# Optimization experiments

Measured on AMD Instinct MI355X. Metric: run time of the kernel, lower is better.

## Reference

```python
import jax, jax.numpy as jnp
import numpy as np

NUM_HEADS = 8
MASK_RATE = 0.5


def setup_inputs() -> dict:
    key = jax.random.key(0)
    ks = jax.random.split(key, 6)
    B, N, C = 8, 1024, 256
    TABLE = 10
    att_embedding = jax.random.normal(ks[0], (B, N, C), dtype=jnp.float32)
    relation_position = jax.random.randint(ks[1], (B, N, N), 0, TABLE, dtype=jnp.int32)
    rel_len = jax.random.randint(ks[2], (B,), 0, 20, dtype=jnp.int32)
    W_qkv = jax.random.normal(ks[3], (C, 3 * C), dtype=jnp.float32) * (1.0 / np.sqrt(C))
    W_proj = jax.random.normal(ks[4], (C, C), dtype=jnp.float32) * (1.0 / np.sqrt(C))
    b_proj = jnp.zeros((C,), dtype=jnp.float32)
    bias_table = jax.random.normal(ks[5], (TABLE, NUM_HEADS), dtype=jnp.float32) * 0.02
    return {
        "att_embedding": att_embedding,
        "relation_position": relation_position,
        "rel_len": rel_len,
        "W_qkv": W_qkv,
        "W_proj": W_proj,
        "b_proj": b_proj,
        "bias_table": bias_table,
    }


def reference(att_embedding, relation_position, rel_len, W_qkv, W_proj, b_proj, bias_table):
    B, N, C = att_embedding.shape
    H = NUM_HEADS
    hd = C // H
    scale = hd ** -0.5

    # QKV projection (no bias): [B,N,3C] -> q,k,v each [B,H,N,hd]
    qkv = (att_embedding @ W_qkv).reshape(B, N, 3, H, hd)
    qkv = jnp.transpose(qkv, (2, 0, 3, 1, 4))
    q, k, v = qkv[0], qkv[1], qkv[2]

    # Attention scores [B,H,N,N]
    attn = jnp.einsum("bhnd,bhmd->bhnm", q, k) * scale

    # Relative position bias: gather [B,N,N,H] -> [B,H,N,N]
    pos_bias = jnp.transpose(bias_table[relation_position], (0, 3, 1, 2))

    # Mask bias: table row t gets -100 iff t > mask_len (mask_len+1 .. TABLE-1);
    # identical across heads -> compute as [B,1,N,N] instead of materializing [B,H,N,N].
    mask_len = (rel_len.astype(jnp.float32) * MASK_RATE).astype(jnp.int32)
    mask_bias = jnp.where(relation_position > mask_len[:, None, None], -100.0, 0.0)[:, None]

    attn = jax.nn.softmax(attn + pos_bias + mask_bias, axis=-1)

    # Weighted values -> [B,N,C] -> output projection
    x = jnp.einsum("bhnm,bhmd->bnhd", attn, v).reshape(B, N, C)
    x = x @ W_proj + b_proj
    return x
```

## Files before the change

### kernel.cpp

```cpp
#include <hip/hip_runtime.h>
#include <hip/hip_bf16.h>

typedef __bf16 bf16;
typedef __bf16 bf16x2 __attribute__((ext_vector_type(2)));
typedef __bf16 bf16x8 __attribute__((ext_vector_type(8)));
typedef float f32x4 __attribute__((ext_vector_type(4)));
typedef int i32x4 __attribute__((ext_vector_type(4)));

#define B_ 8
#define N_ 1024
#define C_ 256
#define H_ 8
#define C3_ 768
#define QS 0.25500398f
#define FMAX 16.0f


__global__ __launch_bounds__(256) void prep(
    const float* __restrict__ Wqkv, const float* __restrict__ Wproj,
    bf16* __restrict__ Wq_tiled, bf16* __restrict__ Wp_tiled)
{
  int bb = blockIdx.x;
  int o = bb * 256 + threadIdx.x;
  if (bb < 768) {
    int kk = o & 31;
    int idx = o >> 5;
    int nr = idx & 63;
    int qq = idx >> 6;
    int nt = qq % 12, kt = qq / 12;
    int n = nt * 64 + nr, k = kt * 32 + kk;
    Wq_tiled[o] = (bf16)Wqkv[k * C3_ + n];
  } else {
    int p = o - 768 * 256;
    int kk = p & 31;
    int n = (p >> 5) & 255;
    int kt = p >> 13;
    int k = kt * 32 + kk;
    Wp_tiled[p] = (bf16)Wproj[k * C_ + n];
  }
}

__global__ __launch_bounds__(256) void gemm_qkv(
    const float* __restrict__ A, const bf16* __restrict__ Wq_tiled,
    bf16* __restrict__ q, bf16* __restrict__ kT, bf16* __restrict__ vT)
{
  __shared__ bf16 As[128][40];
  __shared__ bf16 Bts[128][40];
  __shared__ bf16 Vls[64][136];

  int tid = threadIdx.x;
  int wave = tid >> 6, lane = tid & 63, quad = lane >> 4, l16 = lane & 15;
  int m0 = blockIdx.x * 128, n0 = blockIdx.y * 128;
  int msub = (wave & 1) * 64, nsub = (wave >> 1) * 64;

  f32x4 acc[4][4] = {};

  int arow = tid >> 1, akc = (tid & 1) * 16;
  const float* aptr = A + (long)(m0 + arow) * C_ + akc;
  int bn = tid >> 1, bkc = (tid & 1) * 16;
  const bf16* bptr = Wq_tiled +
      ((long)(blockIdx.y * 2 + (bn >> 6)) * 2048 + (bn & 63) * 32 + bkc);

  float4 a0 = *reinterpret_cast<const float4*>(aptr);
  float4 a1 = *reinterpret_cast<const float4*>(aptr + 4);
  float4 a2 = *reinterpret_cast<const float4*>(aptr + 8);
  float4 a3 = *reinterpret_cast<const float4*>(aptr + 12);
  i32x4 bv0 = *reinterpret_cast<const i32x4*>(bptr);
  i32x4 bv1 = *reinterpret_cast<const i32x4*>(bptr + 8);

  for (int kt = 0; kt < 8; ++kt) {
    __syncthreads();
    {
      bf16 at[16] = {(bf16)a0.x, (bf16)a0.y, (bf16)a0.z, (bf16)a0.w,
                     (bf16)a1.x, (bf16)a1.y, (bf16)a1.z, (bf16)a1.w,
                     (bf16)a2.x, (bf16)a2.y, (bf16)a2.z, (bf16)a2.w,
                     (bf16)a3.x, (bf16)a3.y, (bf16)a3.z, (bf16)a3.w};
      *reinterpret_cast<bf16x8*>(&As[arow][akc]) = *reinterpret_cast<bf16x8*>(at);
      *reinterpret_cast<bf16x8*>(&As[arow][akc + 8]) = *reinterpret_cast<bf16x8*>(at + 8);
      *reinterpret_cast<i32x4*>(&Bts[bn][bkc]) = bv0;
      *reinterpret_cast<i32x4*>(&Bts[bn][bkc + 8]) = bv1;
    }
    __syncthreads();

    if (kt < 7) {
      int kn = (kt + 1) * 32;
      a0 = *reinterpret_cast<const float4*>(aptr + kn);
      a1 = *reinterpret_cast<const float4*>(aptr + kn + 4);
      a2 = *reinterpret_cast<const float4*>(aptr + kn + 8);
      a3 = *reinterpret_cast<const float4*>(aptr + kn + 12);
      bv0 = *reinterpret_cast<const i32x4*>(bptr + (long)(kt + 1) * 24576);
      bv1 = *reinterpret_cast<const i32x4*>(bptr + (long)(kt + 1) * 24576 + 8);
    }

    bf16x8 af[4], bfr[4];
#pragma unroll
    for (int mi = 0; mi < 4; ++mi)
      af[mi] = *reinterpret_cast<const bf16x8*>(&As[msub + mi * 16 + l16][quad * 8]);
#pragma unroll
    for (int ni = 0; ni < 4; ++ni)
      bfr[ni] = *reinterpret_cast<const bf16x8*>(&Bts[nsub + ni * 16 + l16][quad * 8]);
#pragma unroll
    for (int mi = 0; mi < 4; ++mi)
#pragma unroll
      for (int ni = 0; ni < 4; ++ni)
        acc[mi][ni] = __builtin_amdgcn_mfma_f32_16x16x32_bf16(af[mi], bfr[ni], acc[mi][ni], 0, 0, 0);
  }

  if (n0 < 256) {
#pragma unroll
    for (int mi = 0; mi < 4; ++mi)
#pragma unroll
      for (int ni = 0; ni < 4; ++ni)
#pragma unroll
        for (int r = 0; r < 4; ++r) {
          int row = m0 + msub + mi * 16 + quad * 4 + r;
          int col = n0 + nsub + ni * 16 + l16;
          q[(long)row * 256 + col] = (bf16)(acc[mi][ni][r] * QS);
        }
  } else if (n0 < 512) {
#pragma unroll
    for (int mi = 0; mi < 4; ++mi)
#pragma unroll
      for (int ni = 0; ni < 4; ++ni)
#pragma unroll
        for (int r = 0; r < 4; ++r) {
          int row = m0 + msub + mi * 16 + quad * 4 + r;
          int c = n0 + nsub + ni * 16 + l16 - 256;
          int b = row >> 10, n = row & 1023;
          int h = c >> 5, d = c & 31;
          kT[(((long)(b * H_ + h)) * N_ + n) * 32 + d] = (bf16)acc[mi][ni][r];
        }
  } else {
    int b = m0 >> 10;
#pragma unroll
    for (int ch = 0; ch < 2; ++ch) {
      __syncthreads();
      if ((nsub >> 6) == ch) {
#pragma unroll
        for (int mi = 0; mi < 4; ++mi)
#pragma unroll
          for (int ni = 0; ni < 4; ++ni)
#pragma unroll
            for (int r = 0; r < 4; ++r) {
              int cc = ni * 16 + l16;
              int nn = msub + mi * 16 + quad * 4 + r;
              int np = (nn & 96) | (2 * (nn & 15)) | ((nn >> 4) & 1);
              Vls[cc][np] = (bf16)acc[mi][ni][r];
            }
      }
      __syncthreads();
      int cc = tid >> 2, nseg = (tid & 3) * 32;
      long base = ((long)(b * C_ + (n0 - 512) + ch * 64 + cc)) * N_ + (m0 & 1023) + nseg;
#pragma unroll
      for (int j = 0; j < 4; ++j)
        *reinterpret_cast<i32x4*>(vT + base + j * 8) =
            *reinterpret_cast<const i32x4*>(&Vls[cc][nseg + j * 8]);
    }
  }
}

__global__ __launch_bounds__(512) void flash_attn(
    const bf16* __restrict__ q, const bf16* __restrict__ kT,
    const bf16* __restrict__ vT, const int* __restrict__ rel,
    const int* __restrict__ rel_len, const float* __restrict__ btab,
    const bf16* __restrict__ Wp_tiled, const float* __restrict__ bias,
    float* __restrict__ out)
{
  __shared__ bf16 Vs[H_][32][40];
  __shared__ bf16 Pls[H_][16 * 40];
  __shared__ float btlq[4][H_][17];
  __shared__ bf16 attL[16][264];

  int tid = threadIdx.x;
  int h = tid >> 6, lane = tid & 63, quad = lane >> 4, l16 = lane & 15;
  int b = blockIdx.y, i0 = blockIdx.x * 16;
  long bN = (long)b * N_;

  int mask_len = (int)((float)rel_len[b] * 0.5f);
  if (tid < 320) {
    int cp = tid / 80, rem = tid % 80, t = rem >> 3, hh = rem & 7;
    btlq[cp][hh][t] =
        (btab[t * H_ + hh] + (t > mask_len ? -100.f : 0.f) - FMAX) * 1.44269504f;
  }
  __syncthreads();

  bf16x8 qf = *reinterpret_cast<const bf16x8*>(
      q + (bN + i0 + l16) * 256 + h * 32 + quad * 8);

  const bf16* kbase = kT + ((long)(b * H_ + h)) * N_ * 32 + quad * 8;
  int vrl = lane >> 1, voff = (lane & 1) * 16;
  const bf16* vgp = vT + ((long)b * C_ + h * 32 + vrl) * N_ + voff;
  const int* relr = rel + (bN + i0 + quad * 4) * N_ + l16;

  bf16x8 kf0 = *reinterpret_cast<const bf16x8*>(kbase + (long)l16 * 32);
  bf16x8 kf1 = *reinterpret_cast<const bf16x8*>(kbase + (long)(16 + l16) * 32);
  bf16x8 vr0 = *reinterpret_cast<const bf16x8*>(vgp);
  bf16x8 vr1 = *reinterpret_cast<const bf16x8*>(vgp + 8);
  int rv[8];
#pragma unroll
  for (int r = 0; r < 4; ++r) {
    rv[r] = relr[(long)r * N_];
    rv[4 + r] = relr[(long)r * N_ + 16];
  }

  f32x4 oacc[2] = {};
  float l_part[4] = {0.f, 0.f, 0.f, 0.f};

  for (int j0 = 0; j0 < N_; j0 += 32) {
    *reinterpret_cast<bf16x8*>(&Vs[h][vrl][voff]) = vr0;
    *reinterpret_cast<bf16x8*>(&Vs[h][vrl][voff + 8]) = vr1;

    int jn = j0 + 32; jn = (jn < N_) ? jn : 0;
    bf16x8 kn0 = *reinterpret_cast<const bf16x8*>(kbase + (long)(jn + l16) * 32);
    bf16x8 kn1 = *reinterpret_cast<const bf16x8*>(kbase + (long)(jn + 16 + l16) * 32);
    bf16x8 vn0 = *reinterpret_cast<const bf16x8*>(vgp + jn);
    bf16x8 vn1 = *reinterpret_cast<const bf16x8*>(vgp + jn + 8);
    int rn[8];
#pragma unroll
    for (int r = 0; r < 4; ++r) {
      rn[r] = relr[(long)r * N_ + jn];
      rn[4 + r] = relr[(long)r * N_ + jn + 16];
    }

    f32x4 z = {};
    f32x4 s0 = __builtin_amdgcn_mfma_f32_16x16x32_bf16(qf, kf0, z, 0, 0, 0);
    f32x4 s1 = __builtin_amdgcn_mfma_f32_16x16x32_bf16(qf, kf1, z, 0, 0, 0);
    kf0 = kn0; kf1 = kn1;

#pragma unroll
    for (int r = 0; r < 4; ++r) {
      int il = quad * 4 + r;
      float p0 = exp2f(s0[r] + btlq[quad][h][rv[r]]);
      float p1 = exp2f(s1[r] + btlq[quad][h][rv[4 + r]]);
      l_part[r] += p0 + p1;
      bf16x2 pp = {(bf16)p0, (bf16)p1};
      *reinterpret_cast<bf16x2*>(&Pls[h][il * 40 + l16 * 2]) = pp;
    }
#pragma unroll
    for (int t = 0; t < 8; ++t) rv[t] = rn[t];

    asm volatile("s_waitcnt lgkmcnt(0)" ::: "memory");
    bf16x8 pf = *reinterpret_cast<const bf16x8*>(&Pls[h][l16 * 40 + quad * 8]);
    bf16x8 vf0 = *reinterpret_cast<const bf16x8*>(&Vs[h][l16][quad * 8]);
    bf16x8 vf1 = *reinterpret_cast<const bf16x8*>(&Vs[h][16 + l16][quad * 8]);
    oacc[0] = __builtin_amdgcn_mfma_f32_16x16x32_bf16(pf, vf0, oacc[0], 0, 0, 0);
    oacc[1] = __builtin_amdgcn_mfma_f32_16x16x32_bf16(pf, vf1, oacc[1], 0, 0, 0);

    vr0 = vn0; vr1 = vn1;
  }

#pragma unroll
  for (int r = 0; r < 4; ++r) {
    float l = l_part[r];
#pragma unroll
    for (int m = 1; m < 16; m <<= 1) l += __shfl_xor(l, m);
    float inv = 1.f / l;
    attL[quad * 4 + r][h * 32 + l16] = (bf16)(oacc[0][r] * inv);
    attL[quad * 4 + r][h * 32 + 16 + l16] = (bf16)(oacc[1][r] * inv);
  }
  __syncthreads();

  f32x4 pacc[2] = {};
  const bf16* wp = Wp_tiled + ((h * 32 + l16) * 32 + quad * 8);
#pragma unroll
  for (int kt = 0; kt < 8; ++kt) {
    bf16x8 afr = *reinterpret_cast<const bf16x8*>(&attL[l16][kt * 32 + quad * 8]);
    bf16x8 b0 = *reinterpret_cast<const bf16x8*>(wp + kt * 8192);
    bf16x8 b1 = *reinterpret_cast<const bf16x8*>(wp + kt * 8192 + 512);
    pacc[0] = __builtin_amdgcn_mfma_f32_16x16x32_bf16(afr, b0, pacc[0], 0, 0, 0);
    pacc[1] = __builtin_amdgcn_mfma_f32_16x16x32_bf16(afr, b1, pacc[1], 0, 0, 0);
  }
  float bi0 = bias[h * 32 + l16];
  float bi1 = bias[h * 32 + 16 + l16];
#pragma unroll
  for (int r = 0; r < 4; ++r) {
    long rowoff = (bN + i0 + quad * 4 + r) * C_ + h * 32;
    out[rowoff + l16] = pacc[0][r] + bi0;
    out[rowoff + 16 + l16] = pacc[1][r] + bi1;
  }
}

extern "C" void kernel_launch(void* const* d_in, const int* in_sizes, int n_in,
                              void* d_out, int out_size, void* d_ws, size_t ws_size,
                              hipStream_t stream) {
  const float* X     = (const float*)d_in[0];
  const int*   rel   = (const int*)d_in[1];
  const int*   rlen  = (const int*)d_in[2];
  const float* Wqkv  = (const float*)d_in[3];
  const float* Wproj = (const float*)d_in[4];
  const float* bproj = (const float*)d_in[5];
  const float* btab  = (const float*)d_in[6];
  float* out = (float*)d_out;

  char* ws = (char*)d_ws;
  bf16* Wq_tiled = (bf16*)ws;
  bf16* Wp_tiled = (bf16*)(ws + 393216);
  bf16* q  = (bf16*)(ws + 524288);
  bf16* kT = (bf16*)(ws + 524288 + 4194304);
  bf16* vT = (bf16*)(ws + 524288 + 2 * 4194304);

  prep<<<dim3(1024), 256, 0, stream>>>(Wqkv, Wproj, Wq_tiled, Wp_tiled);
  gemm_qkv<<<dim3(8192 / 128, C3_ / 128), 256, 0, stream>>>(X, Wq_tiled, q, kT, vT);
  flash_attn<<<dim3(N_ / 16, B_), 512, 0, stream>>>(
      q, kT, vT, rel, rlen, btab, Wp_tiled, bproj, out);
}
```

Before: 152.8 us.

## Share relation-position tile across heads via packed LDS and widen KV step to 64

Previously each of the 8 head-warps loaded the same relation_position int32 values from global memory. Now 128 threads load the 16x64 tile once per step, pack four row indices into bytes, and share them through LDS. The kernel also stages V for all heads cooperatively with the whole block and moves to 64-key steps split into two 32-key sub-tiles, which halves the loop trip count. The cost is two block-wide barriers per iteration where the old loop had none, plus more LDS and registers.

```diff
diff --git a/kernel.cpp b/kernel.cpp
--- a/kernel.cpp
+++ b/kernel.cpp
@@ -166,7 +166,8 @@
     const bf16* __restrict__ Wp_tiled, const float* __restrict__ bias,
     float* __restrict__ out)
 {
-  __shared__ bf16 Vs[H_][32][40];
+  __shared__ bf16 Vs[2][256][40];
+  __shared__ unsigned RelsP[2][4][33];
   __shared__ bf16 Pls[H_][16 * 40];
   __shared__ float btlq[4][H_][17];
   __shared__ bf16 attL[16][264];
@@ -182,71 +183,93 @@
     btlq[cp][hh][t] =
         (btab[t * H_ + hh] + (t > mask_len ? -100.f : 0.f) - FMAX) * 1.44269504f;
   }
-  __syncthreads();
 
   bf16x8 qf = *reinterpret_cast<const bf16x8*>(
       q + (bN + i0 + l16) * 256 + h * 32 + quad * 8);
 
   const bf16* kbase = kT + ((long)(b * H_ + h)) * N_ * 32 + quad * 8;
-  int vrl = lane >> 1, voff = (lane & 1) * 16;
-  const bf16* vgp = vT + ((long)b * C_ + h * 32 + vrl) * N_ + voff;
-  const int* relr = rel + (bN + i0 + quad * 4) * N_ + l16;
+  int vrow = tid >> 1, voff = (tid & 1) * 16;
+  const bf16* vgp = vT + ((long)b * C_ + vrow) * N_ + voff;
+  int rg = (tid >> 5) & 3, rcol = tid & 31;
+  const int* rgp = rel + (bN + i0 + rg * 4) * N_ + rcol;
 
   bf16x8 kf0 = *reinterpret_cast<const bf16x8*>(kbase + (long)l16 * 32);
   bf16x8 kf1 = *reinterpret_cast<const bf16x8*>(kbase + (long)(16 + l16) * 32);
-  bf16x8 vr0 = *reinterpret_cast<const bf16x8*>(vgp);
-  bf16x8 vr1 = *reinterpret_cast<const bf16x8*>(vgp + 8);
-  int rv[8];
-#pragma unroll
-  for (int r = 0; r < 4; ++r) {
-    rv[r] = relr[(long)r * N_];
-    rv[4 + r] = relr[(long)r * N_ + 16];
+  bf16x8 kf2 = *reinterpret_cast<const bf16x8*>(kbase + (long)(32 + l16) * 32);
+  bf16x8 kf3 = *reinterpret_cast<const bf16x8*>(kbase + (long)(48 + l16) * 32);
+  bf16x8 vrA0 = *reinterpret_cast<const bf16x8*>(vgp);
+  bf16x8 vrA1 = *reinterpret_cast<const bf16x8*>(vgp + 8);
+  bf16x8 vrB0 = *reinterpret_cast<const bf16x8*>(vgp + 32);
+  bf16x8 vrB1 = *reinterpret_cast<const bf16x8*>(vgp + 40);
+  unsigned rrA = 0, rrB = 0;
+  if (tid < 128) {
+    rrA = ((unsigned)(rgp[0] & 255)) | ((unsigned)(rgp[N_] & 255) << 8) |
+          ((unsigned)(rgp[2 * N_] & 255) << 16) | ((unsigned)(rgp[3 * N_] & 255) << 24);
+    rrB = ((unsigned)(rgp[32] & 255)) | ((unsigned)(rgp[N_ + 32] & 255) << 8) |
+          ((unsigned)(rgp[2 * N_ + 32] & 255) << 16) | ((unsigned)(rgp[3 * N_ + 32] & 255) << 24);
   }
 
   f32x4 oacc[2] = {};
   float l_part[4] = {0.f, 0.f, 0.f, 0.f};
 
-  for (int j0 = 0; j0 < N_; j0 += 32) {
-    *reinterpret_cast<bf16x8*>(&Vs[h][vrl][voff]) = vr0;
-    *reinterpret_cast<bf16x8*>(&Vs[h][vrl][voff + 8]) = vr1;
-
-    int jn = j0 + 32; jn = (jn < N_) ? jn : 0;
+  for (int jt = 0; jt < 16; ++jt) {
+    __syncthreads();
+    *reinterpret_cast<bf16x8*>(&Vs[0][vrow][voff]) = vrA0;
+    *reinterpret_cast<bf16x8*>(&Vs[0][vrow][voff + 8]) = vrA1;
+    *reinterpret_cast<bf16x8*>(&Vs[1][vrow][voff]) = vrB0;
+    *reinterpret_cast<bf16x8*>(&Vs[1][vrow][voff + 8]) = vrB1;
+    if (tid < 128) {
+      RelsP[0][rg][rcol] = rrA;
+      RelsP[1][rg][rcol] = rrB;
+    }
+    __syncthreads();
+
+    int jn = (jt + 1) * 64; jn = (jn < N_) ? jn : 0;
     bf16x8 kn0 = *reinterpret_cast<const bf16x8*>(kbase + (long)(jn + l16) * 32);
     bf16x8 kn1 = *reinterpret_cast<const bf16x8*>(kbase + (long)(jn + 16 + l16) * 32);
-    bf16x8 vn0 = *reinterpret_cast<const bf16x8*>(vgp + jn);
-    bf16x8 vn1 = *reinterpret_cast<const bf16x8*>(vgp + jn + 8);
-    int rn[8];
-#pragma unroll
-    for (int r = 0; r < 4; ++r) {
-      rn[r] = relr[(long)r * N_ + jn];
-      rn[4 + r] = relr[(long)r * N_ + jn + 16];
-    }
-
-    f32x4 z = {};
-    f32x4 s0 = __builtin_amdgcn_mfma_f32_16x16x32_bf16(qf, kf0, z, 0, 0, 0);
-    f32x4 s1 = __builtin_amdgcn_mfma_f32_16x16x32_bf16(qf, kf1, z, 0, 0, 0);
-    kf0 = kn0; kf1 = kn1;
-
-#pragma unroll
-    for (int r = 0; r < 4; ++r) {
-      int il = quad * 4 + r;
-      float p0 = exp2f(s0[r] + btlq[quad][h][rv[r]]);
-      float p1 = exp2f(s1[r] + btlq[quad][h][rv[4 + r]]);
-      l_part[r] += p0 + p1;
-      bf16x2 pp = {(bf16)p0, (bf16)p1};
-      *reinterpret_cast<bf16x2*>(&Pls[h][il * 40 + l16 * 2]) = pp;
-    }
-#pragma unroll
-    for (int t = 0; t < 8; ++t) rv[t] = rn[t];
-
-    asm volatile("s_waitcnt lgkmcnt(0)" ::: "memory");
-    bf16x8 pf = *reinterpret_cast<const bf16x8*>(&Pls[h][l16 * 40 + quad * 8]);
-    bf16x8 vf0 = *reinterpret_cast<const bf16x8*>(&Vs[h][l16][quad * 8]);
-    bf16x8 vf1 = *reinterpret_cast<const bf16x8*>(&Vs[h][16 + l16][quad * 8]);
-    oacc[0] = __builtin_amdgcn_mfma_f32_16x16x32_bf16(pf, vf0, oacc[0], 0, 0, 0);
-    oacc[1] = __builtin_amdgcn_mfma_f32_16x16x32_bf16(pf, vf1, oacc[1], 0, 0, 0);
-
-    vr0 = vn0; vr1 = vn1;
+    bf16x8 kn2 = *reinterpret_cast<const bf16x8*>(kbase + (long)(jn + 32 + l16) * 32);
+    bf16x8 kn3 = *reinterpret_cast<const bf16x8*>(kbase + (long)(jn + 48 + l16) * 32);
+    vrA0 = *reinterpret_cast<const bf16x8*>(vgp + jn);
+    vrA1 = *reinterpret_cast<const bf16x8*>(vgp + jn + 8);
+    vrB0 = *reinterpret_cast<const bf16x8*>(vgp + jn + 32);
+    vrB1 = *reinterpret_cast<const bf16x8*>(vgp + jn + 40);
+    if (tid < 128) {
+      rrA = ((unsigned)(rgp[jn] & 255)) | ((unsigned)(rgp[N_ + jn] & 255) << 8) |
+            ((unsigned)(rgp[2 * N_ + jn] & 255) << 16) | ((unsigned)(rgp[3 * N_ + jn] & 255) << 24);
+      rrB = ((unsigned)(rgp[jn + 32] & 255)) | ((unsigned)(rgp[N_ + jn + 32] & 255) << 8) |
+            ((unsigned)(rgp[2 * N_ + jn + 32] & 255) << 16) | ((unsigned)(rgp[3 * N_ + jn + 32] & 255) << 24);
+    }
+
+#pragma unroll
+    for (int sub = 0; sub < 2; ++sub) {
+      bf16x8 ka = sub ? kf2 : kf0;
+      bf16x8 kb = sub ? kf3 : kf1;
+      f32x4 z = {};
+      f32x4 s0 = __builtin_amdgcn_mfma_f32_16x16x32_bf16(qf, ka, z, 0, 0, 0);
+      f32x4 s1 = __builtin_amdgcn_mfma_f32_16x16x32_bf16(qf, kb, z, 0, 0, 0);
+
+      unsigned w0 = RelsP[sub][quad][l16];
+      unsigned w1 = RelsP[sub][quad][16 + l16];
+#pragma unroll
+      for (int r = 0; r < 4; ++r) {
+        int il = quad * 4 + r;
+        int rv0 = (w0 >> (8 * r)) & 255;
+        int rv1 = (w1 >> (8 * r)) & 255;
+        float p0 = exp2f(s0[r] + btlq[quad][h][rv0]);
+        float p1 = exp2f(s1[r] + btlq[quad][h][rv1]);
+        l_part[r] += p0 + p1;
+        bf16x2 pp = {(bf16)p0, (bf16)p1};
+        *reinterpret_cast<bf16x2*>(&Pls[h][il * 40 + l16 * 2]) = pp;
+      }
+      asm volatile("s_waitcnt lgkmcnt(0)" ::: "memory");
+      bf16x8 pf = *reinterpret_cast<const bf16x8*>(&Pls[h][l16 * 40 + quad * 8]);
+      bf16x8 vf0 = *reinterpret_cast<const bf16x8*>(&Vs[sub][h * 32 + l16][quad * 8]);
+      bf16x8 vf1 = *reinterpret_cast<const bf16x8*>(&Vs[sub][h * 32 + 16 + l16][quad * 8]);
+      oacc[0] = __builtin_amdgcn_mfma_f32_16x16x32_bf16(pf, vf0, oacc[0], 0, 0, 0);
+      oacc[1] = __builtin_amdgcn_mfma_f32_16x16x32_bf16(pf, vf1, oacc[1], 0, 0, 0);
+    }
+
+    kf0 = kn0; kf1 = kn1; kf2 = kn2; kf3 = kn3;
   }
 
 #pragma unroll
```

Result: no change. 150.0 us (-1.8%).
